# Performance work log

Hardware: AMD Instinct MI355X
Metric: run time of the kernel (lower is better)

The kernel has to match this reference:

```python
import jax, jax.numpy as jnp
import numpy as np

B, T, N_EMBD, HEAD_SIZE = 4, 4096, 32, 32


def setup_inputs() -> dict:
    key = jax.random.key(0)
    k1, k2, k3, k4 = jax.random.split(key, 4)
    x = jax.random.normal(k1, (B, T, N_EMBD), dtype=jnp.float32)
    Wq = jax.random.normal(k2, (HEAD_SIZE, N_EMBD), dtype=jnp.float32) * (N_EMBD ** -0.5)
    Wk = jax.random.normal(k3, (HEAD_SIZE, N_EMBD), dtype=jnp.float32) * (N_EMBD ** -0.5)
    Wv = jax.random.normal(k4, (HEAD_SIZE, N_EMBD), dtype=jnp.float32) * (N_EMBD ** -0.5)
    return {"x": x, "Wq": Wq, "Wk": Wk, "Wv": Wv}


def reference(x, Wq, Wk, Wv):
    # Linear(bias=False): y = x @ W.T  -> [B, T, head_size]
    q = jnp.einsum('btn,hn->bth', x, Wq)
    k = jnp.einsum('btn,hn->bth', x, Wk)
    v = jnp.einsum('btn,hn->bth', x, Wv)
    scale = q.shape[-1] ** -0.5
    # [B, T, T] attention scores
    wei = jnp.einsum('bth,bsh->bts', q, k) * scale
    # Faithful to source: tril the scores, then mask entries equal to 0
    tril = jnp.tril(wei)
    wei = jax.nn.softmax(jnp.where(tril == 0, -jnp.inf, tril), axis=-1)
    return jnp.einsum('bts,bsh->bth', wei, v)
```

## Files before the change

kernel.cpp:

```cpp
#include <hip/hip_runtime.h>
#include <cmath>

#define BB 4
#define TT 4096
#define NE 32
#define HS 32

#define IPB 2176
#define MAXSP 16
#define SLOT 288
#define FNEG (-1.0e30f)
#define BIAS 6.0f
#define SC2  0.25506953149031156f

typedef unsigned int uint32;
typedef __fp16 half2v __attribute__((ext_vector_type(2)));
typedef __fp16 half4v __attribute__((ext_vector_type(4)));
typedef __fp16 half8v __attribute__((ext_vector_type(8)));
typedef float f32x4 __attribute__((ext_vector_type(4)));

__device__ __forceinline__ half2v u2h(uint32 u) {
    union { uint32 u; half2v h; } x; x.u = u; return x.h;
}

#if __has_builtin(__builtin_amdgcn_cvt_pkrtz)
__device__ __forceinline__ half2v pkf16(float a, float b) {
    return __builtin_amdgcn_cvt_pkrtz(a, b);
}
#else
__device__ __forceinline__ half2v pkf16(float a, float b) {
    half2v h; h.x = (__fp16)a; h.y = (__fp16)b; return h;
}
#endif

__global__ __launch_bounds__(256) void qkv_proj(
    const float* __restrict__ x,
    const float* __restrict__ Wq,
    const float* __restrict__ Wk,
    const float* __restrict__ Wv,
    __fp16* __restrict__ Qh, __fp16* __restrict__ Kh,
    __fp16* __restrict__ Vt8)
{
    int tid = blockIdx.x * 256 + threadIdx.x;
    int row = tid >> 5;
    int h   = tid & 31;
    const float4* xr4 = reinterpret_cast<const float4*>(x + (size_t)row * NE);
    float4 xv4[8];
    #pragma unroll
    for (int k = 0; k < 8; ++k) xv4[k] = xr4[k];
    const float* xv = (const float*)xv4;
    float aq = 0.f, ak = 0.f, av = 0.f;
    #pragma unroll
    for (int d = 0; d < NE; ++d) {
        aq = fmaf(xv[d], Wq[h * NE + d], aq);
        ak = fmaf(xv[d], Wk[h * NE + d], ak);
        av = fmaf(xv[d], Wv[h * NE + d], av);
    }
    size_t o = (size_t)row * HS + h;
    Qh[o] = (__fp16)(aq * SC2);
    Kh[o] = (__fp16)ak;
    int b = row >> 12, t = row & (TT - 1);
    Vt8[((size_t)(b * (TT / 4) + (t >> 2)) * 16 + (h & 15)) * 8
        + (h >> 4) * 4 + (t & 3)] = (__fp16)av;
}

__global__ __launch_bounds__(256, 6) void attn_partial(
    const __fp16* __restrict__ Qh, const __fp16* __restrict__ Kh,
    const __fp16* __restrict__ Vt8, float* __restrict__ part)
{
    int wave = threadIdx.x >> 6;
    int lane = threadIdx.x & 63;
    int item = blockIdx.x * 4 + wave;
    int b = item / IPB;
    int r = item - b * IPB;
    int g = (int)((sqrtf((float)(4 + 2 * r)) - 2.0f) * 0.25f);
    if (g < 0) g = 0;
    while (8 * (g + 1) * (g + 2) <= r) ++g;
    while (8 * g * (g + 1) > r) --g;
    int rr = r - 8 * g * (g + 1);
    int tq = rr / (g + 1);
    int t  = 16 * g + tq;
    int sp = rr - tq * (g + 1);
    int qt0 = t * 16;
    int kbase = sp * 256;
    int kend  = min(kbase + 256, qt0 + 16);
    int nsub  = (kend - kbase) >> 4;

    int c = lane & 15;
    int q = lane >> 4;

    const __fp16* Qb = Qh  + (size_t)b * TT * HS;
    const __fp16* Kb = Kh  + (size_t)b * TT * HS;
    const __fp16* Vb = Vt8 + (size_t)b * (TT / 4) * 128;

    union U4H8  { uint4 u; half8v h; };
    union U4H44 { uint4 u; half4v h4[2]; };
    union H4    { half4v h4; half2v h2[2]; };
    union H4U4  { half2v h[4]; uint4 u; };

    U4H8 qf; qf.u = *(const uint4*)(Qb + (size_t)(qt0 + c) * HS + 8 * q);

    const f32x4 cbias = {-BIAS, -BIAS, -BIAS, -BIAS};
    float l0 = 0.f, l1 = 0.f;
    f32x4 oa0 = {0.f,0.f,0.f,0.f}, oa1 = oa0, ob0 = oa0, ob1 = oa0;

    auto do16 = [&](int kb, float& l, f32x4& o0, f32x4& o1) {
        U4H8 kf; kf.u = *(const uint4*)(Kb + (size_t)(kb + c) * HS + 8 * q);
        U4H44 vf; vf.u = *(const uint4*)(Vb + (size_t)((kb >> 2) + q) * 128 + c * 8);
        f32x4 s = __builtin_amdgcn_mfma_f32_16x16x32_f16(kf.h, qf.h, cbias, 0, 0, 0);
        bool diag = (kb == qt0);
        float w[4];
        #pragma unroll
        for (int j = 0; j < 4; ++j) {
            w[j] = (s[j] != -BIAS) ? s[j] : FNEG;
            if (diag && (4 * q + j > c)) w[j] = FNEG;
        }
        float p0 = exp2f(w[0]), p1 = exp2f(w[1]);
        float p2 = exp2f(w[2]), p3 = exp2f(w[3]);
        l += (p0 + p1) + (p2 + p3);
        H4 pf; pf.h2[0] = pkf16(p0, p1); pf.h2[1] = pkf16(p2, p3);
        o0 = __builtin_amdgcn_mfma_f32_16x16x16f16(vf.h4[0], pf.h4, o0, 0, 0, 0);
        o1 = __builtin_amdgcn_mfma_f32_16x16x16f16(vf.h4[1], pf.h4, o1, 0, 0, 0);
    };

    if (nsub == 16) {
        #pragma unroll 2
        for (int i = 0; i < 8; ++i) {
            do16(kbase + 32 * i,      l0, oa0, oa1);
            do16(kbase + 32 * i + 16, l1, ob0, ob1);
        }
    } else {
        int i = 0;
        for (; i + 1 < nsub; i += 2) {
            do16(kbase + 16 * i,      l0, oa0, oa1);
            do16(kbase + 16 * i + 16, l1, ob0, ob1);
        }
        if (i < nsub) do16(kbase + 16 * i, l0, oa0, oa1);
    }

    float l = l0 + l1;
    f32x4 o0, o1;
    #pragma unroll
    for (int k = 0; k < 4; ++k) {
        o0[k] = oa0[k] + ob0[k];
        o1[k] = oa1[k] + ob1[k];
    }

    float lt = l + __shfl_xor(l, 16);
    lt += __shfl_xor(lt, 32);

    float* P = part + (size_t)((b * 256 + t) * MAXSP + sp) * SLOT;
    if (q == 0) P[16 + c] = lt;
    H4U4 a;
    a.h[0] = pkf16(o0[0], o0[1]); a.h[1] = pkf16(o0[2], o0[3]);
    a.h[2] = pkf16(o1[0], o1[1]); a.h[3] = pkf16(o1[2], o1[3]);
    *((uint4*)((uint32*)(P + 32) + c * 16 + q * 4)) = a.u;
}

__global__ __launch_bounds__(256) void attn_combine(
    const float* __restrict__ part, float* __restrict__ out)
{
    int tid = blockIdx.x * 256 + threadIdx.x;
    int hq = tid & 3;
    int c  = (tid >> 2) & 15;
    int t  = (tid >> 6) & 255;
    int b  = tid >> 14;
    int ns = (t >> 4) + 1;

    const float* base = part + (size_t)(b * 256 + t) * MAXSP * SLOT;

    float acc[8];
    #pragma unroll
    for (int k = 0; k < 8; ++k) acc[k] = 0.f;
    float L = 0.f;
    for (int s = 0; s < ns; ++s) {
        const float* P = base + (size_t)s * SLOT;
        L += P[16 + c];
        uint4 ov = *(const uint4*)((const uint32*)(P + 32) + c * 16 + 4 * hq);
        const uint32* ovp = (const uint32*)&ov;
        #pragma unroll
        for (int pr = 0; pr < 4; ++pr) {
            half2v hh = u2h(ovp[pr]);
            acc[2 * pr]     += (float)hh.x;
            acc[2 * pr + 1] += (float)hh.y;
        }
    }
    float invL = 1.0f / L;
    float* orow = out + ((size_t)(b * TT + t * 16 + c)) * HS;
    float4 w0 = {acc[0] * invL, acc[1] * invL, acc[2] * invL, acc[3] * invL};
    float4 w1 = {acc[4] * invL, acc[5] * invL, acc[6] * invL, acc[7] * invL};
    *(float4*)(orow + 4 * hq) = w0;
    *(float4*)(orow + 16 + 4 * hq) = w1;
}

extern "C" void kernel_launch(void* const* d_in, const int* in_sizes, int n_in,
                              void* d_out, int out_size, void* d_ws, size_t ws_size,
                              hipStream_t stream)
{
    const float* x  = (const float*)d_in[0];
    const float* Wq = (const float*)d_in[1];
    const float* Wk = (const float*)d_in[2];
    const float* Wv = (const float*)d_in[3];
    float* out = (float*)d_out;

    __fp16* Qh  = (__fp16*)d_ws;
    __fp16* Kh  = Qh + (size_t)BB * TT * HS;
    __fp16* Vt8 = Kh + (size_t)BB * TT * HS;
    float* part = (float*)(Vt8 + (size_t)BB * TT * HS);

    qkv_proj<<<dim3((BB * TT * HS) / 256), dim3(256), 0, stream>>>(
        x, Wq, Wk, Wv, Qh, Kh, Vt8);
    attn_partial<<<dim3((BB * IPB) / 4), dim3(256), 0, stream>>>(
        Qh, Kh, Vt8, part);
    attn_combine<<<dim3(256), dim3(256), 0, stream>>>(part, out);
}
```

Baseline: 114.0 us.

## Process two 16-row query tiles per wave, sharing K/V loads, with separate diagonal masking

Each wave now handles a 32-query block (two 16-row Q fragments), so every K and V fragment it loads feeds four PV MFMAs and two QK MFMAs instead of half as many. This halves K/V global loads per unit of work and halves the number of work items. The causal mask is applied only in the last two key sub-blocks, so the main loop drops the per-step diagonal check. Register pressure rises, which is why the occupancy hint drops from 6 to 4 blocks, and fewer items may leave the load less balanced across CUs.

```diff
diff --git a/kernel.cpp b/kernel.cpp
--- a/kernel.cpp
+++ b/kernel.cpp
@@ -6,7 +6,7 @@
 #define NE 32
 #define HS 32
 
-#define IPB 2176
+#define IPB2 1088
 #define MAXSP 16
 #define SLOT 288
 #define FNEG (-1.0e30f)
@@ -64,27 +64,29 @@
         + (h >> 4) * 4 + (t & 3)] = (__fp16)av;
 }
 
-__global__ __launch_bounds__(256, 6) void attn_partial(
+__global__ __launch_bounds__(256, 4) void attn_partial(
     const __fp16* __restrict__ Qh, const __fp16* __restrict__ Kh,
     const __fp16* __restrict__ Vt8, float* __restrict__ part)
 {
     int wave = threadIdx.x >> 6;
     int lane = threadIdx.x & 63;
     int item = blockIdx.x * 4 + wave;
-    int b = item / IPB;
-    int r = item - b * IPB;
-    int g = (int)((sqrtf((float)(4 + 2 * r)) - 2.0f) * 0.25f);
+    int b = item / IPB2;
+    int r = item - b * IPB2;
+    int g = (int)((sqrtf((float)(1 + r)) - 1.0f) * 0.5f);
     if (g < 0) g = 0;
-    while (8 * (g + 1) * (g + 2) <= r) ++g;
-    while (8 * g * (g + 1) > r) --g;
-    int rr = r - 8 * g * (g + 1);
+    while (4 * (g + 1) * (g + 2) <= r) ++g;
+    while (4 * g * (g + 1) > r) --g;
+    int rr = r - 4 * g * (g + 1);
     int tq = rr / (g + 1);
-    int t  = 16 * g + tq;
+    int tt = 8 * g + tq;
     int sp = rr - tq * (g + 1);
-    int qt0 = t * 16;
+    int qt0 = tt * 32;
     int kbase = sp * 256;
-    int kend  = min(kbase + 256, qt0 + 16);
+    int kend  = min(kbase + 256, qt0 + 32);
     int nsub  = (kend - kbase) >> 4;
+    bool hasdiag = (kend == qt0 + 32);
+    int nfast = nsub - (hasdiag ? 2 : 0);
 
     int c = lane & 15;
     int q = lane >> 4;
@@ -98,63 +100,79 @@
     union H4    { half4v h4; half2v h2[2]; };
     union H4U4  { half2v h[4]; uint4 u; };
 
-    U4H8 qf; qf.u = *(const uint4*)(Qb + (size_t)(qt0 + c) * HS + 8 * q);
+    U4H8 qf0; qf0.u = *(const uint4*)(Qb + (size_t)(qt0 + c) * HS + 8 * q);
+    U4H8 qf1; qf1.u = *(const uint4*)(Qb + (size_t)(qt0 + 16 + c) * HS + 8 * q);
 
     const f32x4 cbias = {-BIAS, -BIAS, -BIAS, -BIAS};
     float l0 = 0.f, l1 = 0.f;
-    f32x4 oa0 = {0.f,0.f,0.f,0.f}, oa1 = oa0, ob0 = oa0, ob1 = oa0;
-
-    auto do16 = [&](int kb, float& l, f32x4& o0, f32x4& o1) {
+    f32x4 o00 = {0.f,0.f,0.f,0.f}, o01 = o00, o10 = o00, o11 = o00;
+
+    auto dofast = [&](int kb) {
         U4H8 kf; kf.u = *(const uint4*)(Kb + (size_t)(kb + c) * HS + 8 * q);
         U4H44 vf; vf.u = *(const uint4*)(Vb + (size_t)((kb >> 2) + q) * 128 + c * 8);
-        f32x4 s = __builtin_amdgcn_mfma_f32_16x16x32_f16(kf.h, qf.h, cbias, 0, 0, 0);
-        bool diag = (kb == qt0);
-        float w[4];
+        f32x4 s0 = __builtin_amdgcn_mfma_f32_16x16x32_f16(kf.h, qf0.h, cbias, 0, 0, 0);
+        f32x4 s1 = __builtin_amdgcn_mfma_f32_16x16x32_f16(kf.h, qf1.h, cbias, 0, 0, 0);
+        float p0[4], p1[4];
         #pragma unroll
         for (int j = 0; j < 4; ++j) {
-            w[j] = (s[j] != -BIAS) ? s[j] : FNEG;
-            if (diag && (4 * q + j > c)) w[j] = FNEG;
+            p0[j] = exp2f((s0[j] != -BIAS) ? s0[j] : FNEG);
+            p1[j] = exp2f((s1[j] != -BIAS) ? s1[j] : FNEG);
         }
-        float p0 = exp2f(w[0]), p1 = exp2f(w[1]);
-        float p2 = exp2f(w[2]), p3 = exp2f(w[3]);
-        l += (p0 + p1) + (p2 + p3);
-        H4 pf; pf.h2[0] = pkf16(p0, p1); pf.h2[1] = pkf16(p2, p3);
-        o0 = __builtin_amdgcn_mfma_f32_16x16x16f16(vf.h4[0], pf.h4, o0, 0, 0, 0);
-        o1 = __builtin_amdgcn_mfma_f32_16x16x16f16(vf.h4[1], pf.h4, o1, 0, 0, 0);
+        l0 += (p0[0] + p0[1]) + (p0[2] + p0[3]);
+        l1 += (p1[0] + p1[1]) + (p1[2] + p1[3]);
+        H4 pf0; pf0.h2[0] = pkf16(p0[0], p0[1]); pf0.h2[1] = pkf16(p0[2], p0[3]);
+        H4 pf1; pf1.h2[0] = pkf16(p1[0], p1[1]); pf1.h2[1] = pkf16(p1[2], p1[3]);
+        o00 = __builtin_amdgcn_mfma_f32_16x16x16f16(vf.h4[0], pf0.h4, o00, 0, 0, 0);
+        o01 = __builtin_amdgcn_mfma_f32_16x16x16f16(vf.h4[1], pf0.h4, o01, 0, 0, 0);
+        o10 = __builtin_amdgcn_mfma_f32_16x16x16f16(vf.h4[0], pf1.h4, o10, 0, 0, 0);
+        o11 = __builtin_amdgcn_mfma_f32_16x16x16f16(vf.h4[1], pf1.h4, o11, 0, 0, 0);
     };
 
-    if (nsub == 16) {
-        #pragma unroll 2
-        for (int i = 0; i < 8; ++i) {
-            do16(kbase + 32 * i,      l0, oa0, oa1);
-            do16(kbase + 32 * i + 16, l1, ob0, ob1);
+    auto domask = [&](int kb) {
+        U4H8 kf; kf.u = *(const uint4*)(Kb + (size_t)(kb + c) * HS + 8 * q);
+        U4H44 vf; vf.u = *(const uint4*)(Vb + (size_t)((kb >> 2) + q) * 128 + c * 8);
+        f32x4 s0 = __builtin_amdgcn_mfma_f32_16x16x32_f16(kf.h, qf0.h, cbias, 0, 0, 0);
+        f32x4 s1 = __builtin_amdgcn_mfma_f32_16x16x32_f16(kf.h, qf1.h, cbias, 0, 0, 0);
+        int r0 = kb - qt0 + 4 * q;
+        int r1 = r0 - 16;
+        float p0[4], p1[4];
+        #pragma unroll
+        for (int j = 0; j < 4; ++j) {
+            float w0 = (s0[j] != -BIAS) ? s0[j] : FNEG;
+            float w1 = (s1[j] != -BIAS) ? s1[j] : FNEG;
+            if (r0 + j > c) w0 = FNEG;
+            if (r1 + j > c) w1 = FNEG;
+            p0[j] = exp2f(w0);
+            p1[j] = exp2f(w1);
         }
-    } else {
-        int i = 0;
-        for (; i + 1 < nsub; i += 2) {
-            do16(kbase + 16 * i,      l0, oa0, oa1);
-            do16(kbase + 16 * i + 16, l1, ob0, ob1);
-        }
-        if (i < nsub) do16(kbase + 16 * i, l0, oa0, oa1);
-    }
-
-    float l = l0 + l1;
-    f32x4 o0, o1;
-    #pragma unroll
-    for (int k = 0; k < 4; ++k) {
-        o0[k] = oa0[k] + ob0[k];
-        o1[k] = oa1[k] + ob1[k];
-    }
-
-    float lt = l + __shfl_xor(l, 16);
-    lt += __shfl_xor(lt, 32);
-
-    float* P = part + (size_t)((b * 256 + t) * MAXSP + sp) * SLOT;
-    if (q == 0) P[16 + c] = lt;
+        l0 += (p0[0] + p0[1]) + (p0[2] + p0[3]);
+        l1 += (p1[0] + p1[1]) + (p1[2] + p1[3]);
+        H4 pf0; pf0.h2[0] = pkf16(p0[0], p0[1]); pf0.h2[1] = pkf16(p0[2], p0[3]);
+        H4 pf1; pf1.h2[0] = pkf16(p1[0], p1[1]); pf1.h2[1] = pkf16(p1[2], p1[3]);
+        o00 = __builtin_amdgcn_mfma_f32_16x16x16f16(vf.h4[0], pf0.h4, o00, 0, 0, 0);
+        o01 = __builtin_amdgcn_mfma_f32_16x16x16f16(vf.h4[1], pf0.h4, o01, 0, 0, 0);
+        o10 = __builtin_amdgcn_mfma_f32_16x16x16f16(vf.h4[0], pf1.h4, o10, 0, 0, 0);
+        o11 = __builtin_amdgcn_mfma_f32_16x16x16f16(vf.h4[1], pf1.h4, o11, 0, 0, 0);
+    };
+
+    int kb = kbase;
+    #pragma unroll 2
+    for (int i = 0; i < nfast; ++i) { dofast(kb); kb += 16; }
+    if (hasdiag) { domask(kb); domask(kb + 16); }
+
+    float lt0 = l0 + __shfl_xor(l0, 16); lt0 += __shfl_xor(lt0, 32);
+    float lt1 = l1 + __shfl_xor(l1, 16); lt1 += __shfl_xor(lt1, 32);
+
+    float* P0 = part + (size_t)((b * 256 + 2 * tt) * MAXSP + sp) * SLOT;
+    float* P1 = P0 + (size_t)MAXSP * SLOT;
+    if (q == 0) { P0[16 + c] = lt0; P1[16 + c] = lt1; }
     H4U4 a;
-    a.h[0] = pkf16(o0[0], o0[1]); a.h[1] = pkf16(o0[2], o0[3]);
-    a.h[2] = pkf16(o1[0], o1[1]); a.h[3] = pkf16(o1[2], o1[3]);
-    *((uint4*)((uint32*)(P + 32) + c * 16 + q * 4)) = a.u;
+    a.h[0] = pkf16(o00[0], o00[1]); a.h[1] = pkf16(o00[2], o00[3]);
+    a.h[2] = pkf16(o01[0], o01[1]); a.h[3] = pkf16(o01[2], o01[3]);
+    *((uint4*)((uint32*)(P0 + 32) + c * 16 + q * 4)) = a.u;
+    a.h[0] = pkf16(o10[0], o10[1]); a.h[1] = pkf16(o10[2], o10[3]);
+    a.h[2] = pkf16(o11[0], o11[1]); a.h[3] = pkf16(o11[2], o11[3]);
+    *((uint4*)((uint32*)(P1 + 32) + c * 16 + q * 4)) = a.u;
 }
 
 __global__ __launch_bounds__(256) void attn_combine(
@@ -210,7 +228,7 @@
 
     qkv_proj<<<dim3((BB * TT * HS) / 256), dim3(256), 0, stream>>>(
         x, Wq, Wk, Wv, Qh, Kh, Vt8);
-    attn_partial<<<dim3((BB * IPB) / 4), dim3(256), 0, stream>>>(
+    attn_partial<<<dim3((BB * IPB2) / 4), dim3(256), 0, stream>>>(
         Qh, Kh, Vt8, part);
     attn_combine<<<dim3(256), dim3(256), 0, stream>>>(part, out);
 }
```

New measurement: 112.5 us. About the same (-1.3%).
